# Kernel optimization log

Measured on AMD Instinct MI355X. Metric: run time of the kernel, lower is better.

The kernel has to match this reference:

```python
import jax, jax.numpy as jnp
import numpy as np
from math import sqrt

FACTOR = 5

def setup_inputs() -> dict:
    key = jax.random.key(0)
    kq, kk, kv, ka = jax.random.split(key, 4)
    B, L, H, D = 4, 2048, 8, 64
    return {
        "queries": jax.random.normal(kq, (B, L, H, D), dtype=jnp.float32),
        "keys": jax.random.normal(kk, (B, L, H, D), dtype=jnp.float32),
        "values": jax.random.normal(kv, (B, L, H, D), dtype=jnp.float32),
        "atten_data": jax.random.normal(ka, (B, L, 2), dtype=jnp.float32),
        "attn_mask": jnp.zeros((1,), dtype=bool),  # unused (mask_flag=False)
    }

def reference(queries, keys, values, atten_data, attn_mask):
    # layer_num=1, mask_flag=False, output_attention=False, scale=None
    B, L_Q, H, D = queries.shape
    L_K = keys.shape[1]
    U_part = min(FACTOR * int(np.ceil(np.log(L_K))), L_K)  # sample_k
    u = min(FACTOR * int(np.ceil(np.log(L_Q))), L_Q)       # n_top

    Q = jnp.transpose(queries, (0, 2, 1, 3))  # [B,H,L_Q,D]
    K = jnp.transpose(keys, (0, 2, 1, 3))     # [B,H,L_K,D]
    V = jnp.transpose(values, (0, 2, 1, 3))   # [B,H,L_V,D]

    # --- _prob_QK: random K sampling per query position ---
    index_sample = jax.random.randint(jax.random.key(42), (L_Q, U_part), 0, L_K)
    K_sample = K[:, :, index_sample, :]                      # [B,H,L_Q,U_part,D]
    Q_K_sample = jnp.einsum("bhld,bhlsd->bhls", Q, K_sample)  # [B,H,L_Q,U_part]
    M = Q_K_sample.max(axis=-1) - Q_K_sample.sum(axis=-1) / L_K  # [B,H,L_Q]
    _, M_top = jax.lax.top_k(M, u)                           # [B,H,u]

    Q_reduce = jnp.take_along_axis(Q, M_top[..., None], axis=2)  # [B,H,u,D]
    scores_top = jnp.einsum("bhud,bhkd->bhuk", Q_reduce, K)      # [B,H,u,L_K]

    scale = 1.0 / sqrt(D)
    scores_top = scores_top * scale

    # --- initial context: mean of V broadcast over L_Q (mask_flag=False) ---
    V_mean = V.mean(axis=-2, keepdims=True)                  # [B,H,1,D]
    context = jnp.broadcast_to(V_mean, (B, H, L_Q, D))

    # --- update context at top-u query positions ---
    attn = jax.nn.softmax(scores_top, axis=-1)               # [B,H,u,L_K]
    upd = jnp.einsum("bhuk,bhkd->bhud", attn, V)             # [B,H,u,D]
    bidx = jnp.arange(B)[:, None, None]
    hidx = jnp.arange(H)[None, :, None]
    context = context.at[bidx, hidx, M_top].set(upd)

    return jnp.transpose(context, (0, 2, 1, 3))  # [B,L_Q,H,D]
```

## Files before the change

### kernel.cpp

```cpp
#include <hip/hip_runtime.h>
#include <math.h>

#define B_  4
#define L_  2048
#define H_  8
#define D_  64
#define U_  40
#define HD  (H_*D_)

#define WS_NEED_KC16 5600256
#define WS_NEED_KC8  2937856

struct U2 { unsigned a, b; };

__host__ __device__ constexpr unsigned rotl32c(unsigned x, int r){
  return (x<<r)|(x>>(32-r));
}

__host__ __device__ constexpr U2 tf2x32(unsigned k0, unsigned k1,
                                        unsigned x0, unsigned x1)
{
  const unsigned k2 = k0 ^ k1 ^ 0x1BD11BDAu;
  const int rA[4] = {13,15,26,6};
  const int rB[4] = {17,29,16,24};
  x0 += k0; x1 += k1;
  for (int i=0;i<4;i++){ x0+=x1; x1=rotl32c(x1,rA[i]); x1^=x0; }
  x0 += k1; x1 += k2 + 1u;
  for (int i=0;i<4;i++){ x0+=x1; x1=rotl32c(x1,rB[i]); x1^=x0; }
  x0 += k2; x1 += k0 + 2u;
  for (int i=0;i<4;i++){ x0+=x1; x1=rotl32c(x1,rA[i]); x1^=x0; }
  x0 += k0; x1 += k1 + 3u;
  for (int i=0;i<4;i++){ x0+=x1; x1=rotl32c(x1,rB[i]); x1^=x0; }
  x0 += k1; x1 += k2 + 4u;
  for (int i=0;i<4;i++){ x0+=x1; x1=rotl32c(x1,rA[i]); x1^=x0; }
  x0 += k2; x1 += k0 + 5u;
  return U2{x0, x1};
}

__global__ __launch_bounds__(256) void mvm_kernel(const float* __restrict__ q,
                                                  const float* __restrict__ k,
                                                  const float* __restrict__ v,
                                                  float* __restrict__ M,
                                                  float* __restrict__ vmean)
{
  int tid = threadIdx.x;
  int w = tid >> 6, lane = tid & 63;

  if (blockIdx.x < 512){
    int g = blockIdx.x;
    int bh = g & 31, chunk = g >> 5;
    int b = bh >> 3, h = bh & 7;
    int l0 = chunk*128 + w*32;
    float s = 0.f;
    for (int i=0;i<32;i++)
      s += v[(size_t)(b*L_ + l0 + i)*HD + h*D_ + lane];
    atomicAdd(&vmean[bh*D_ + lane], s);
    return;
  }

  int g    = blockIdx.x - 512;
  int b    = g & 3;
  int lblk = g >> 2;
  int l    = lblk*4 + w;
  int h    = lane >> 3, d8 = lane & 7;

  const float* qrow = q + (size_t)(b*L_ + l)*HD;
  float4 q0 = *(const float4*)(qrow + lane*8);
  float4 q1 = *(const float4*)(qrow + lane*8 + 4);

  constexpr U2 K2 = tf2x32(0u, 42u, 0u, 1u);
  int myidx = 0;
  if (lane < U_){
    U2 r = tf2x32(K2.a, K2.b, 0u, (unsigned)(l*U_ + lane));
    myidx = (int)((r.a ^ r.b) & 2047u);
  }

  const float* kb = k + (size_t)b*L_*HD;
  float vmax = -INFINITY, vsum = 0.f;
  #pragma unroll 8
  for (int s=0;s<U_;s++){
    int kidx = __shfl(myidx, s, 64);
    const float* kr = kb + (size_t)kidx*HD;
    float4 k0 = *(const float4*)(kr + lane*8);
    float4 k1 = *(const float4*)(kr + lane*8 + 4);
    float p = q0.x*k0.x + q0.y*k0.y + q0.z*k0.z + q0.w*k0.w
            + q1.x*k1.x + q1.y*k1.y + q1.z*k1.z + q1.w*k1.w;
    p += __shfl_xor(p, 1, 64);
    p += __shfl_xor(p, 2, 64);
    p += __shfl_xor(p, 4, 64);
    vmax = fmaxf(vmax, p);
    vsum += p;
  }
  if (d8 == 0)
    M[(b*8 + h)*L_ + l] = vmax - vsum * (1.0f/(float)L_);
}

__global__ __launch_bounds__(256) void topk_init_kernel(const float* __restrict__ M,
                                                        const float* __restrict__ vmean,
                                                        int*   __restrict__ mtop,
                                                        float* __restrict__ out)
{
  int tid = threadIdx.x;

  if (blockIdx.x >= 32){
    int i = (blockIdx.x - 32)*256 + tid;
    int d4 = i & 15;
    int h  = (i >> 4) & 7;
    int bl = i >> 7;
    int b  = bl >> 11;
    float4 vm = ((const float4*)(vmean + (b*H_ + h)*D_))[d4];
    const float sc = 1.0f/(float)L_;
    float4 o; o.x = vm.x*sc; o.y = vm.y*sc; o.z = vm.z*sc; o.w = vm.w*sc;
    ((float4*)out)[i] = o;
    return;
  }

  __shared__ unsigned keys[L_];
  __shared__ unsigned hist[256];
  __shared__ unsigned sh_prefix, sh_need, sh_cgt, sh_ceq;
  int bh = blockIdx.x;

  #pragma unroll
  for (int i=0;i<8;i++){
    unsigned bits = __float_as_uint(M[bh*L_ + tid + 256*i]);
    keys[tid + 256*i] = (bits & 0x80000000u) ? ~bits : (bits | 0x80000000u);
  }
  if (tid == 0){ sh_prefix = 0u; sh_need = U_; sh_cgt = 0u; sh_ceq = 0u; }

  unsigned pmask = 0u;
  for (int p = 3; p >= 0; --p){
    hist[tid] = 0u;
    __syncthreads();
    unsigned pref = sh_prefix;
    #pragma unroll
    for (int i=0;i<8;i++){
      unsigned key = keys[tid + 256*i];
      if ((key & pmask) == pref)
        atomicAdd(&hist[(key >> (8*p)) & 255u], 1u);
    }
    __syncthreads();

    if (tid < 64){
      unsigned h0 = hist[tid*4+0], h1 = hist[tid*4+1];
      unsigned h2 = hist[tid*4+2], h3 = hist[tid*4+3];
      unsigned loc = h0+h1+h2+h3;
      unsigned s = loc;
      #pragma unroll
      for (int off=1; off<64; off<<=1){
        unsigned o = __shfl_down(s, off, 64);
        if (tid + off < 64) s += o;
      }
      unsigned need = sh_need;
      unsigned cum = s - loc;
      unsigned bsel = 0xFFFFFFFFu, nn = 0u;
      if (cum < need && cum + h3 >= need){ bsel = tid*4+3; nn = need - cum; }
      cum += h3;
      if (bsel==0xFFFFFFFFu && cum < need && cum + h2 >= need){ bsel = tid*4+2; nn = need - cum; }
      cum += h2;
      if (bsel==0xFFFFFFFFu && cum < need && cum + h1 >= need){ bsel = tid*4+1; nn = need - cum; }
      cum += h1;
      if (bsel==0xFFFFFFFFu && cum < need && cum + h0 >= need){ bsel = tid*4+0; nn = need - cum; }
      if (bsel != 0xFFFFFFFFu){
        sh_prefix = sh_prefix | (bsel << (8*p));
        sh_need = nn;
      }
    }
    __syncthreads();
    pmask |= 0xFFu << (8*p);
  }

  unsigned K40 = sh_prefix;
  unsigned need = sh_need;
  #pragma unroll
  for (int i=0;i<8;i++){
    int idx = tid + 256*i;
    unsigned key = keys[idx];
    if (key > K40){
      unsigned pos = atomicAdd(&sh_cgt, 1u);
      mtop[bh*U_ + pos] = idx;
    } else if (key == K40){
      unsigned e = atomicAdd(&sh_ceq, 1u);
      if (e < need) mtop[bh*U_ + (U_ - need) + e] = idx;
    }
  }
}

__global__ __launch_bounds__(256, 3) void attn_kernel(const float* __restrict__ q,
                                                      const float* __restrict__ k,
                                                      const float* __restrict__ v,
                                                      const int*   __restrict__ mtop,
                                                      float* __restrict__ pacc,
                                                      float* __restrict__ pl,
                                                      int nt, int KC)
{
  __shared__ float sh[128*68 + 40*64];
  float* Kt  = sh;
  float* Qs  = sh + 128*68;
  float* psQ = sh;

  int g  = blockIdx.x;
  int bh = g & 31, kc = g >> 5;
  int b = bh >> 3, h = bh & 7;
  int tid = threadIdx.x, w = tid >> 6, lane = tid & 63;

  #pragma unroll
  for (int c=0;c<3;c++){
    int flat = c*256 + tid;
    if (flat < 640){
      int row = flat >> 4, col = flat & 15;
      int lstar = mtop[bh*U_ + row];
      ((float4*)(Qs + row*64))[col] =
        ((const float4*)(q + (size_t)(b*L_ + lstar)*HD + h*D_))[col];
    }
  }

  float acc[10], lsum[10];
  #pragma unroll
  for (int qq=0;qq<10;qq++){ acc[qq] = 0.f; lsum[qq] = 0.f; }

  for (int tt=0; tt<nt; ++tt){
    int kt = (kc*nt + tt)*128;
    if (tt) __syncthreads();
    #pragma unroll
    for (int c=0;c<8;c++){
      int flat = c*256 + tid;
      int row = flat >> 4, col = flat & 15;
      ((float4*)(Kt + row*68))[col] =
        ((const float4*)(k + (size_t)(b*L_ + kt + row)*HD + h*D_))[col];
    }
    __syncthreads();

    float s0[10], s1[10];
    #pragma unroll
    for (int qq=0;qq<10;qq++){ s0[qq] = 0.f; s1[qq] = 0.f; }
    const float* kr0 = Kt + lane*68;
    const float* kr1 = Kt + (lane+64)*68;
    #pragma unroll
    for (int t=0;t<16;t++){
      float4 k0 = ((const float4*)kr0)[t];
      float4 k1 = ((const float4*)kr1)[t];
      #pragma unroll
      for (int qq=0;qq<10;qq++){
        float4 qf = ((const float4*)(Qs + (w*10+qq)*64))[t];
        s0[qq] += k0.x*qf.x + k0.y*qf.y + k0.z*qf.z + k0.w*qf.w;
        s1[qq] += k1.x*qf.x + k1.y*qf.y + k1.z*qf.z + k1.w*qf.w;
      }
    }
    __syncthreads();

    #pragma unroll
    for (int qq=0;qq<10;qq++){
      float p0 = __expf(s0[qq]*0.125f);
      float p1 = __expf(s1[qq]*0.125f);
      psQ[(w*10+qq)*128 + lane]      = p0;
      psQ[(w*10+qq)*128 + lane + 64] = p1;
      lsum[qq] += p0 + p1;
    }

    const float* vb = v + (size_t)(b*L_ + kt)*HD + h*D_ + lane;
    #pragma unroll 4
    for (int k4=0;k4<32;k4++){
      float v0 = vb[(size_t)(4*k4+0)*HD];
      float v1 = vb[(size_t)(4*k4+1)*HD];
      float v2 = vb[(size_t)(4*k4+2)*HD];
      float v3 = vb[(size_t)(4*k4+3)*HD];
      #pragma unroll
      for (int qq=0;qq<10;qq++){
        float4 pp = ((const float4*)(psQ + (w*10+qq)*128))[k4];
        acc[qq] += pp.x*v0 + pp.y*v1 + pp.z*v2 + pp.w*v3;
      }
    }
  }

  #pragma unroll
  for (int qq=0;qq<10;qq++){
    float ls = lsum[qq];
    #pragma unroll
    for (int off=32; off; off>>=1) ls += __shfl_xor(ls, off, 64);
    int gu = bh*U_ + w*10 + qq;
    pacc[(size_t)(gu*KC + kc)*64 + lane] = acc[qq];
    if (lane == 0) pl[gu*KC + kc] = ls;
  }
}

__global__ __launch_bounds__(256) void combine_kernel(const int* __restrict__ mtop,
                                                      const float* __restrict__ pacc,
                                                      const float* __restrict__ pl,
                                                      float* __restrict__ out,
                                                      int KC)
{
  int gu = blockIdx.x*4 + (threadIdx.x >> 6);
  int lane = threadIdx.x & 63;
  int bh = gu / U_, u = gu - bh*U_;
  float a = 0.f, L = 0.f;
  for (int c=0;c<KC;c++){
    a += pacc[(size_t)(gu*KC + c)*64 + lane];
    L += pl[gu*KC + c];
  }
  int b = bh >> 3, h = bh & 7;
  int lstar = mtop[bh*U_ + u];
  out[(size_t)(b*L_ + lstar)*HD + h*D_ + lane] = a / L;
}

extern "C" void kernel_launch(void* const* d_in, const int* in_sizes, int n_in,
                              void* d_out, int out_size, void* d_ws, size_t ws_size,
                              hipStream_t stream)
{
  const float* q = (const float*)d_in[0];
  const float* k = (const float*)d_in[1];
  const float* v = (const float*)d_in[2];
  float* out = (float*)d_out;

  int KC = (ws_size >= (size_t)WS_NEED_KC16) ? 16 : 8;
  int nt = 16 / KC;

  size_t o_pl    = (size_t)1280*KC*64*4;
  size_t o_vmean = o_pl + (size_t)1280*KC*4;
  size_t o_M     = o_vmean + 2048*4;
  size_t o_mtop  = o_M + 65536*4;

  float* pacc  = (float*)d_ws;
  float* pl    = (float*)((char*)d_ws + o_pl);
  float* vmean = (float*)((char*)d_ws + o_vmean);
  float* M     = (float*)((char*)d_ws + o_M);
  int*   mtop  = (int*)  ((char*)d_ws + o_mtop);

  hipMemsetAsync(vmean, 0, 2048*sizeof(float), stream);
  mvm_kernel      <<<2560,  256, 0, stream>>>(q, k, v, M, vmean);
  topk_init_kernel<<<4128,  256, 0, stream>>>(M, vmean, mtop, out);
  attn_kernel     <<<32*KC, 256, 0, stream>>>(q, k, v, mtop, pacc, pl, nt, KC);
  combine_kernel  <<<320,   256, 0, stream>>>(mtop, pacc, pl, out, KC);
}
```

Measured before the change: 173.0 us.

## Split sampled-K scoring across two waves per query and stage V in LDS

The sparsity-measure kernel now gives each query row two wavefronts, each scoring 20 of the 40 sampled keys, and merges their partial max and sum through shared memory. This doubles the block count and shortens the serial gather chain per wave. The attention kernel also loads each V tile into LDS together with the K tile, so V is read with coalesced float4 loads instead of strided scalar global reads. The larger LDS footprint lowers the occupancy hint from 3 to 2 blocks per CU.

```diff
diff --git a/kernel.cpp b/kernel.cpp
--- a/kernel.cpp
+++ b/kernel.cpp
@@ -9,7 +9,6 @@
 #define HD  (H_*D_)
 
 #define WS_NEED_KC16 5600256
-#define WS_NEED_KC8  2937856
 
 struct U2 { unsigned a, b; };
 
@@ -43,6 +42,7 @@
                                                   float* __restrict__ M,
                                                   float* __restrict__ vmean)
 {
+  __shared__ float red[2][2][8][2];
   int tid = threadIdx.x;
   int w = tid >> 6, lane = tid & 63;
 
@@ -58,11 +58,13 @@
     return;
   }
 
-  int g    = blockIdx.x - 512;
-  int b    = g & 3;
-  int lblk = g >> 2;
-  int l    = lblk*4 + w;
-  int h    = lane >> 3, d8 = lane & 7;
+  int g     = blockIdx.x - 512;
+  int b     = g & 3;
+  int lpair = g >> 2;
+  int ll    = w >> 1;
+  int half  = w & 1;
+  int l     = lpair*2 + ll;
+  int h     = lane >> 3, d8 = lane & 7;
 
   const float* qrow = q + (size_t)(b*L_ + l)*HD;
   float4 q0 = *(const float4*)(qrow + lane*8);
@@ -77,9 +79,9 @@
 
   const float* kb = k + (size_t)b*L_*HD;
   float vmax = -INFINITY, vsum = 0.f;
-  #pragma unroll 8
-  for (int s=0;s<U_;s++){
-    int kidx = __shfl(myidx, s, 64);
+  #pragma unroll 10
+  for (int s=0;s<20;s++){
+    int kidx = __shfl(myidx, half*20 + s, 64);
     const float* kr = kb + (size_t)kidx*HD;
     float4 k0 = *(const float4*)(kr + lane*8);
     float4 k1 = *(const float4*)(kr + lane*8 + 4);
@@ -91,8 +93,14 @@
     vmax = fmaxf(vmax, p);
     vsum += p;
   }
-  if (d8 == 0)
-    M[(b*8 + h)*L_ + l] = vmax - vsum * (1.0f/(float)L_);
+  if (d8 == 0){ red[ll][half][h][0] = vmax; red[ll][half][h][1] = vsum; }
+  __syncthreads();
+  if (half == 0 && d8 == 0){
+    float m2 = red[ll][1][h][0], s2 = red[ll][1][h][1];
+    float fm = fmaxf(vmax, m2);
+    float fs = vsum + s2;
+    M[(b*8 + h)*L_ + l] = fm - fs * (1.0f/(float)L_);
+  }
 }
 
 __global__ __launch_bounds__(256) void topk_init_kernel(const float* __restrict__ M,
@@ -185,7 +193,7 @@
   }
 }
 
-__global__ __launch_bounds__(256, 3) void attn_kernel(const float* __restrict__ q,
+__global__ __launch_bounds__(256, 2) void attn_kernel(const float* __restrict__ q,
                                                       const float* __restrict__ k,
                                                       const float* __restrict__ v,
                                                       const int*   __restrict__ mtop,
@@ -193,9 +201,10 @@
                                                       float* __restrict__ pl,
                                                       int nt, int KC)
 {
-  __shared__ float sh[128*68 + 40*64];
+  __shared__ float sh[128*68 + 128*64 + 40*64];
   float* Kt  = sh;
-  float* Qs  = sh + 128*68;
+  float* Vt  = sh + 128*68;
+  float* Qs  = sh + 128*68 + 128*64;
   float* psQ = sh;
 
   int g  = blockIdx.x;
@@ -227,6 +236,8 @@
       int row = flat >> 4, col = flat & 15;
       ((float4*)(Kt + row*68))[col] =
         ((const float4*)(k + (size_t)(b*L_ + kt + row)*HD + h*D_))[col];
+      ((float4*)(Vt + row*64))[col] =
+        ((const float4*)(v + (size_t)(b*L_ + kt + row)*HD + h*D_))[col];
     }
     __syncthreads();
 
@@ -257,13 +268,12 @@
       lsum[qq] += p0 + p1;
     }
 
-    const float* vb = v + (size_t)(b*L_ + kt)*HD + h*D_ + lane;
     #pragma unroll 4
     for (int k4=0;k4<32;k4++){
-      float v0 = vb[(size_t)(4*k4+0)*HD];
-      float v1 = vb[(size_t)(4*k4+1)*HD];
-      float v2 = vb[(size_t)(4*k4+2)*HD];
-      float v3 = vb[(size_t)(4*k4+3)*HD];
+      float v0 = Vt[(4*k4+0)*64 + lane];
+      float v1 = Vt[(4*k4+1)*64 + lane];
+      float v2 = Vt[(4*k4+2)*64 + lane];
+      float v3 = Vt[(4*k4+3)*64 + lane];
       #pragma unroll
       for (int qq=0;qq<10;qq++){
         float4 pp = ((const float4*)(psQ + (w*10+qq)*128))[k4];
@@ -326,7 +336,7 @@
   int*   mtop  = (int*)  ((char*)d_ws + o_mtop);
 
   hipMemsetAsync(vmean, 0, 2048*sizeof(float), stream);
-  mvm_kernel      <<<2560,  256, 0, stream>>>(q, k, v, M, vmean);
+  mvm_kernel      <<<4608,  256, 0, stream>>>(q, k, v, M, vmean);
   topk_init_kernel<<<4128,  256, 0, stream>>>(M, vmean, mtop, out);
   attn_kernel     <<<32*KC, 256, 0, stream>>>(q, k, v, mtop, pacc, pl, nt, KC);
   combine_kernel  <<<320,   256, 0, stream>>>(mtop, pacc, pl, out, KC);
```

After: 164.1 us. -5.2%, faster.
